# Kernel tuning notes

Measured on AMD Instinct MI355X. Metric: run time of the kernel, lower is better.

The kernel has to match this reference:

```python
import jax, jax.numpy as jnp
import numpy as np

N_NODES = 50000
N_EDGES = 150000
F_IN = 128
D = 512
N_GRAPHS = 256
BN_EPS = 1e-5


def setup_inputs() -> dict:
    key = jax.random.key(0)
    ks = jax.random.split(key, 16)
    x = jax.random.normal(ks[0], (N_NODES, F_IN), dtype=jnp.float32)
    edge_index = jax.random.randint(ks[1], (2, N_EDGES), 0, N_NODES, dtype=jnp.int64)
    batch = jnp.sort(jax.random.randint(ks[2], (N_NODES,), 0, N_GRAPHS, dtype=jnp.int64))
    # layer 1 MLP (F_IN -> D -> D)
    W1a = jax.random.normal(ks[3], (F_IN, D), dtype=jnp.float32) / np.sqrt(F_IN)
    b1a = jnp.zeros((D,), dtype=jnp.float32)
    W1b = jax.random.normal(ks[4], (D, D), dtype=jnp.float32) / np.sqrt(D)
    b1b = jnp.zeros((D,), dtype=jnp.float32)
    # layers 2-5 MLPs (D -> D -> D), stacked on leading axis
    Wa = jax.random.normal(ks[5], (4, D, D), dtype=jnp.float32) / np.sqrt(D)
    ba = jnp.zeros((4, D), dtype=jnp.float32)
    Wb = jax.random.normal(ks[6], (4, D, D), dtype=jnp.float32) / np.sqrt(D)
    bb = jnp.zeros((4, D), dtype=jnp.float32)
    # batchnorm affine params for the 5 BN layers
    gammas = jnp.ones((5, D), dtype=jnp.float32)
    betas = jnp.zeros((5, D), dtype=jnp.float32)
    # final fc
    fcW = jax.random.normal(ks[7], (D, D), dtype=jnp.float32) / np.sqrt(D)
    fcb = jnp.zeros((D,), dtype=jnp.float32)
    return {"x": x, "edge_index": edge_index, "batch": batch,
            "W1a": W1a, "b1a": b1a, "W1b": W1b, "b1b": b1b,
            "Wa": Wa, "ba": ba, "Wb": Wb, "bb": bb,
            "gammas": gammas, "betas": betas, "fcW": fcW, "fcb": fcb}


def _gin_block(x, src, dst, wa, ba_, wb, bb_, gamma, beta):
    # GINConv (eps=0): h_i = x_i + sum_{j->i} x_j, then 2-layer MLP
    agg = jnp.zeros_like(x).at[dst].add(x[src])
    h = x + agg
    h = jnp.maximum(h @ wa + ba_, 0.0) @ wb + bb_
    # outer ReLU then BatchNorm1d (training-mode batch stats, biased var)
    h = jnp.maximum(h, 0.0)
    mean = h.mean(axis=0)
    var = ((h - mean) ** 2).mean(axis=0)
    return gamma * (h - mean) * jax.lax.rsqrt(var + BN_EPS) + beta


def reference(x, edge_index, batch, W1a, b1a, W1b, b1b, Wa, ba, Wb, bb,
              gammas, betas, fcW, fcb):
    src, dst = edge_index[0], edge_index[1]
    h = _gin_block(x, src, dst, W1a, b1a, W1b, b1b, gammas[0], betas[0])
    for i in range(4):
        h = _gin_block(h, src, dst, Wa[i], ba[i], Wb[i], bb[i],
                       gammas[i + 1], betas[i + 1])
    # global mean pool over graphs
    sums = jax.ops.segment_sum(h, batch, num_segments=N_GRAPHS)
    counts = jax.ops.segment_sum(jnp.ones((h.shape[0],), dtype=h.dtype), batch,
                                 num_segments=N_GRAPHS)
    pooled = sums / jnp.maximum(counts, 1.0)[:, None]
    return jnp.tanh(pooled @ fcW + fcb)
```

## Files before the change

### kernel.cpp

```cpp
#include <hip/hip_runtime.h>
#include <math.h>

typedef unsigned short u16;
typedef unsigned int u32;
typedef __attribute__((ext_vector_type(8))) short bf16x8;
typedef __attribute__((ext_vector_type(4))) float f32x4;

__device__ __forceinline__ u16 f2bf(float x) {
    u32 u = __float_as_uint(x);
    return (u16)((u + 0x7FFFu + ((u >> 16) & 1u)) >> 16);
}
__device__ __forceinline__ float bf2f(u16 h) {
    return __uint_as_float(((u32)h) << 16);
}
__device__ __forceinline__ void async16(const void* g, void* l) {
    __builtin_amdgcn_global_load_lds((const __attribute__((address_space(1))) void*)g,
                                     (__attribute__((address_space(3))) void*)l,
                                     16, 0, 0);
}

__device__ __forceinline__ int idx_at(const void* p, long long i, int is64) {
    if (is64) return (int)((const long long*)p)[i];
    return ((const int*)p)[i];
}

__global__ void detect_kernel(const int* __restrict__ ei, int E, int* __restrict__ flag) {
    __shared__ int any;
    if (threadIdx.x == 0) any = 0;
    __syncthreads();
    int n = min(E, 1024);
    for (int i = threadIdx.x; i < n; i += blockDim.x)
        if (ei[2 * i + 1] != 0) any = 1;
    __syncthreads();
    if (threadIdx.x == 0) *flag = (any == 0) ? 1 : 0;
}

__global__ void hist_kernel(const void* __restrict__ idx, long long offs,
                            const int* __restrict__ flag,
                            int* __restrict__ cnt, int n) {
    int is64 = *flag;
    int i = blockIdx.x * blockDim.x + threadIdx.x;
    if (i < n) atomicAdd(&cnt[idx_at(idx, offs + i, is64)], 1);
}

__global__ void scan1_kernel(const int* __restrict__ cnt, int* __restrict__ ofs,
                             int* __restrict__ bsum, int n) {
    __shared__ int s[256];
    int b = blockIdx.x, t = threadIdx.x;
    int base = b * 1024 + t * 4;
    int v0 = (base + 0 < n) ? cnt[base + 0] : 0;
    int v1 = (base + 1 < n) ? cnt[base + 1] : 0;
    int v2 = (base + 2 < n) ? cnt[base + 2] : 0;
    int v3 = (base + 3 < n) ? cnt[base + 3] : 0;
    int tsum = v0 + v1 + v2 + v3;
    s[t] = tsum;
    __syncthreads();
    for (int off = 1; off < 256; off <<= 1) {
        int u = (t >= off) ? s[t - off] : 0;
        __syncthreads();
        s[t] += u;
        __syncthreads();
    }
    int pre = s[t] - tsum;
    int e0 = pre + v0, e1 = e0 + v1, e2 = e1 + v2, e3 = e2 + v3;
    if (base + 0 < n) ofs[base + 1] = e0;
    if (base + 1 < n) ofs[base + 2] = e1;
    if (base + 2 < n) ofs[base + 3] = e2;
    if (base + 3 < n) ofs[base + 4] = e3;
    if (t == 255) bsum[b] = s[255];
    if (b == 0 && t == 0) ofs[0] = 0;
}

__global__ void scan2_kernel(int* __restrict__ bsum, int nb) {
    int t = threadIdx.x;
    int orig = (t < nb) ? bsum[t] : 0;
    int v = orig;
    for (int d = 1; d < 64; d <<= 1) {
        int u = __shfl_up(v, d);
        if (t >= d) v += u;
    }
    if (t < nb) bsum[t] = v - orig;
}

__global__ void scan3_kernel(int* __restrict__ ofs, const int* __restrict__ bsum, int n) {
    int i = blockIdx.x * blockDim.x + threadIdx.x;
    if (i < n) ofs[i + 1] += bsum[i >> 10];
}

__global__ void fill_csr_kernel(const void* __restrict__ ei, long long E,
                                const int* __restrict__ flag,
                                int* __restrict__ cursor, int* __restrict__ esrc, int e) {
    int is64 = *flag;
    int i = blockIdx.x * blockDim.x + threadIdx.x;
    if (i < e) {
        int d = idx_at(ei, E + i, is64);
        int s = idx_at(ei, i, is64);
        int p = atomicAdd(&cursor[d], 1);
        esrc[p] = s;
    }
}

__global__ void copy_int_kernel(const int* __restrict__ a, int* __restrict__ b, int n) {
    int i = blockIdx.x * blockDim.x + threadIdx.x;
    if (i < n) b[i] = a[i];
}

__global__ void aggregate_split_kernel(const float* __restrict__ X,
                                       const int* __restrict__ row_ofs,
                                       const int* __restrict__ esrc,
                                       const float* __restrict__ scale,
                                       const float* __restrict__ shift,
                                       u16* __restrict__ Zhi, u16* __restrict__ Zlo,
                                       int n, int ncols) {
    int tpr = ncols >> 2;
    int nper = 256 / tpr;
    int node = blockIdx.x * nper + threadIdx.x / tpr;
    int c = (threadIdx.x % tpr) * 4;
    if (node >= n) return;
    int beg = row_ofs[node], end = row_ofs[node + 1];
    float4 acc = *reinterpret_cast<const float4*>(X + (size_t)node * ncols + c);
    int e = beg;
    for (; e + 1 < end; e += 2) {
        int s0 = esrc[e], s1 = esrc[e + 1];
        float4 a = *reinterpret_cast<const float4*>(X + (size_t)s0 * ncols + c);
        float4 b = *reinterpret_cast<const float4*>(X + (size_t)s1 * ncols + c);
        acc.x += a.x + b.x; acc.y += a.y + b.y;
        acc.z += a.z + b.z; acc.w += a.w + b.w;
    }
    if (e < end) {
        int s0 = esrc[e];
        float4 a = *reinterpret_cast<const float4*>(X + (size_t)s0 * ncols + c);
        acc.x += a.x; acc.y += a.y; acc.z += a.z; acc.w += a.w;
    }
    if (scale) {
        float d1 = (float)(end - beg + 1);
        float4 sc = *reinterpret_cast<const float4*>(scale + c);
        float4 sh = *reinterpret_cast<const float4*>(shift + c);
        acc.x = sc.x * acc.x + d1 * sh.x;
        acc.y = sc.y * acc.y + d1 * sh.y;
        acc.z = sc.z * acc.z + d1 * sh.z;
        acc.w = sc.w * acc.w + d1 * sh.w;
    }
    ushort4 hv, lv;
    hv.x = f2bf(acc.x); lv.x = f2bf(acc.x - bf2f(hv.x));
    hv.y = f2bf(acc.y); lv.y = f2bf(acc.y - bf2f(hv.y));
    hv.z = f2bf(acc.z); lv.z = f2bf(acc.z - bf2f(hv.z));
    hv.w = f2bf(acc.w); lv.w = f2bf(acc.w - bf2f(hv.w));
    *reinterpret_cast<ushort4*>(Zhi + (size_t)node * ncols + c) = hv;
    *reinterpret_cast<ushort4*>(Zlo + (size_t)node * ncols + c) = lv;
}

__global__ void transpose_split_kernel(const float* __restrict__ W, int K, int N,
                                       u16* __restrict__ Thi, u16* __restrict__ Tlo) {
    __shared__ float t[32][33];
    int k0 = blockIdx.x * 32, n0 = blockIdx.y * 32;
    int tx = threadIdx.x & 31, ty = threadIdx.x >> 5;
#pragma unroll
    for (int i = 0; i < 32; i += 8)
        t[ty + i][tx] = W[(size_t)(k0 + ty + i) * N + n0 + tx];
    __syncthreads();
#pragma unroll
    for (int i = 0; i < 32; i += 8) {
        float v = t[tx][ty + i];
        size_t o = (size_t)(n0 + ty + i) * K + k0 + tx;
        u16 h = f2bf(v);
        Thi[o] = h;
        Tlo[o] = f2bf(v - bf2f(h));
    }
}

struct TBatch {
    const float* src[10];
    u16* dh[10];
    u16* dl[10];
};
__global__ void transpose_split_batch_kernel(TBatch tb) {
    __shared__ float t[32][33];
    int z = blockIdx.z;
    const float* W = tb.src[z];
    u16* Thi = tb.dh[z];
    u16* Tlo = tb.dl[z];
    int k0 = blockIdx.x * 32, n0 = blockIdx.y * 32;
    int tx = threadIdx.x & 31, ty = threadIdx.x >> 5;
#pragma unroll
    for (int i = 0; i < 32; i += 8)
        t[ty + i][tx] = W[(size_t)(k0 + ty + i) * 512 + n0 + tx];
    __syncthreads();
#pragma unroll
    for (int i = 0; i < 32; i += 8) {
        float v = t[tx][ty + i];
        size_t o = (size_t)(n0 + ty + i) * 512 + k0 + tx;
        u16 h = f2bf(v);
        Thi[o] = h;
        Tlo[o] = f2bf(v - bf2f(h));
    }
}

template <int MODE>
__global__ __launch_bounds__(256, 4)
void gemm_mfma(const u16* __restrict__ Ahi, const u16* __restrict__ Alo,
               const u16* __restrict__ Bhi, const u16* __restrict__ Blo,
               const float* __restrict__ bias, int M, int K, int mblk,
               u16* __restrict__ Ohi, u16* __restrict__ Olo,
               float* __restrict__ Of32, float* __restrict__ stats) {
    __shared__ __align__(16) char lds[32768];
    char* ldsAhi = lds;
    char* ldsAlo = lds + 8192;
    char* ldsBhi = lds + 16384;
    char* ldsBlo = lds + 24576;

    const int bid = blockIdx.x;
    const int mt = (bid >> 5) * 8 + (bid & 7);
    const int nb = (bid & 31) >> 3;
    if (mt >= mblk) return;
    const int row0 = mt * 128;
    const int col0 = nb * 128;

    const int tid = threadIdx.x;
    const int lane = tid & 63;
    const int wave = tid >> 6;
    const int wr = wave >> 1, wc = wave & 1;

    f32x4 acc[4][4];
#pragma unroll
    for (int mi = 0; mi < 4; ++mi)
#pragma unroll
        for (int ni = 0; ni < 4; ++ni)
            acc[mi][ni] = (f32x4){0.f, 0.f, 0.f, 0.f};

    const int nkt = K >> 5;
    for (int kt = 0; kt < nkt; ++kt) {
        const int k0 = kt << 5;
#pragma unroll
        for (int i = 0; i < 2; ++i) {
            int c = tid + i * 256;
            int row = c >> 2, s = c & 3;
            int ks = ((s ^ (row & 3)) << 3);
            int ar = row0 + row; if (ar > M - 1) ar = M - 1;
            size_t aoff = (size_t)ar * K + k0 + ks;
            size_t boff = (size_t)(col0 + row) * K + k0 + ks;
            async16(Ahi + aoff, ldsAhi + c * 16);
            async16(Alo + aoff, ldsAlo + c * 16);
            async16(Bhi + boff, ldsBhi + c * 16);
            async16(Blo + boff, ldsBlo + c * 16);
        }
        __syncthreads();
        {
            bf16x8 ah[4], al[4], bh[4], bl[4];
            const int kc = lane >> 4;
#pragma unroll
            for (int mi = 0; mi < 4; ++mi) {
                int ml = wr * 64 + mi * 16 + (lane & 15);
                int off = ml * 64 + ((kc ^ (ml & 3)) << 4);
                ah[mi] = *(const bf16x8*)(ldsAhi + off);
                al[mi] = *(const bf16x8*)(ldsAlo + off);
            }
#pragma unroll
            for (int ni = 0; ni < 4; ++ni) {
                int nl = wc * 64 + ni * 16 + (lane & 15);
                int off = nl * 64 + ((kc ^ (nl & 3)) << 4);
                bh[ni] = *(const bf16x8*)(ldsBhi + off);
                bl[ni] = *(const bf16x8*)(ldsBlo + off);
            }
#pragma unroll
            for (int mi = 0; mi < 4; ++mi)
#pragma unroll
                for (int ni = 0; ni < 4; ++ni) {
                    acc[mi][ni] = __builtin_amdgcn_mfma_f32_16x16x32_bf16(
                        ah[mi], bh[ni], acc[mi][ni], 0, 0, 0);
                    acc[mi][ni] = __builtin_amdgcn_mfma_f32_16x16x32_bf16(
                        ah[mi], bl[ni], acc[mi][ni], 0, 0, 0);
                    acc[mi][ni] = __builtin_amdgcn_mfma_f32_16x16x32_bf16(
                        al[mi], bh[ni], acc[mi][ni], 0, 0, 0);
                }
        }
        __syncthreads();
    }

    const int cl = lane & 15;
    const int rb = (lane >> 4) * 4;
    if (MODE == 0) {
#pragma unroll
        for (int ni = 0; ni < 4; ++ni) {
            int gc = col0 + wc * 64 + ni * 16 + cl;
            float bv = bias[gc];
#pragma unroll
            for (int mi = 0; mi < 4; ++mi) {
                int gr0 = row0 + wr * 64 + mi * 16 + rb;
#pragma unroll
                for (int r = 0; r < 4; ++r) {
                    int gr = gr0 + r;
                    if (gr < M) {
                        float v = fmaxf(acc[mi][ni][r] + bv, 0.f);
                        u16 h = f2bf(v);
                        Ohi[(size_t)gr * 512 + gc] = h;
                        Olo[(size_t)gr * 512 + gc] = f2bf(v - bf2f(h));
                    }
                }
            }
        }
    } else {
#pragma unroll
        for (int ni = 0; ni < 4; ++ni) {
            int gc = col0 + wc * 64 + ni * 16 + cl;
            float bv = bias[gc];
            float s = 0.f, q = 0.f;
#pragma unroll
            for (int mi = 0; mi < 4; ++mi) {
                int gr0 = row0 + wr * 64 + mi * 16 + rb;
#pragma unroll
                for (int r = 0; r < 4; ++r) {
                    int gr = gr0 + r;
                    if (gr < M) {
                        float v = fmaxf(acc[mi][ni][r] + bv, 0.f);
                        Of32[(size_t)gr * 512 + gc] = v;
                        s += v; q += v * v;
                    }
                }
            }
            s += __shfl_xor(s, 16); s += __shfl_xor(s, 32);
            q += __shfl_xor(q, 16); q += __shfl_xor(q, 32);
            if (lane < 16) {
                atomicAdd(&stats[gc], s);
                atomicAdd(&stats[512 + gc], q);
            }
        }
    }
}

__global__ void bn_params_kernel(const float* __restrict__ stats,
                                 const float* __restrict__ gamma,
                                 const float* __restrict__ beta,
                                 float* __restrict__ scale, float* __restrict__ shift,
                                 float invN) {
    int c = blockIdx.x * blockDim.x + threadIdx.x;
    if (c >= 512) return;
    float mean = stats[c] * invN;
    float var = fmaxf(stats[512 + c] * invN - mean * mean, 0.f);
    float a = gamma[c] * rsqrtf(var + 1e-5f);
    scale[c] = a;
    shift[c] = beta[c] - mean * a;
}

#define POOL_ROWS 64
__global__ void pool_kernel(const float* __restrict__ H, const void* __restrict__ batch,
                            const int* __restrict__ flag,
                            float* __restrict__ pooled, int n) {
    int is64 = *flag;
    int c = threadIdx.x * 4;
    int r0 = blockIdx.x * POOL_ROWS;
    if (r0 >= n) return;
    int r1 = min(r0 + POOL_ROWS, n);
    int g = idx_at(batch, r0, is64);
    float4 acc = make_float4(0.f, 0.f, 0.f, 0.f);
    for (int r = r0; r < r1; ++r) {
        int gr = idx_at(batch, r, is64);
        if (gr != g) {
            atomicAdd(&pooled[(size_t)g * 512 + c + 0], acc.x);
            atomicAdd(&pooled[(size_t)g * 512 + c + 1], acc.y);
            atomicAdd(&pooled[(size_t)g * 512 + c + 2], acc.z);
            atomicAdd(&pooled[(size_t)g * 512 + c + 3], acc.w);
            acc = make_float4(0.f, 0.f, 0.f, 0.f);
            g = gr;
        }
        float4 v = *reinterpret_cast<const float4*>(H + (size_t)r * 512 + c);
        acc.x += v.x; acc.y += v.y; acc.z += v.z; acc.w += v.w;
    }
    atomicAdd(&pooled[(size_t)g * 512 + c + 0], acc.x);
    atomicAdd(&pooled[(size_t)g * 512 + c + 1], acc.y);
    atomicAdd(&pooled[(size_t)g * 512 + c + 2], acc.z);
    atomicAdd(&pooled[(size_t)g * 512 + c + 3], acc.w);
}

__global__ void finalize_pool_kernel(const float* __restrict__ pooled,
                                     const int* __restrict__ cg,
                                     const float* __restrict__ scale,
                                     const float* __restrict__ shift,
                                     float* __restrict__ Apool, int total) {
    int idx = blockIdx.x * blockDim.x + threadIdx.x;
    if (idx >= total) return;
    int g = idx >> 9;
    int c = idx & 511;
    float cnt = fmaxf((float)cg[g], 1.f);
    Apool[idx] = scale[c] * (pooled[idx] / cnt) + shift[c];
}

__global__ void fc_tanh_kernel(const float* __restrict__ A,
                               const u16* __restrict__ WThi, const u16* __restrict__ WTlo,
                               const float* __restrict__ bias,
                               float* __restrict__ out, int G) {
    int tm = threadIdx.x >> 6;
    int tn = threadIdx.x & 63;
    int m = blockIdx.x * 4 + tm;
    int n = blockIdx.y * 64 + tn;
    if (m >= G) return;
    const float* a = A + (size_t)m * 512;
    const u16* wh = WThi + (size_t)n * 512;
    const u16* wl = WTlo + (size_t)n * 512;
    float acc = 0.f;
    for (int k = 0; k < 512; k += 4) {
        float4 av = *reinterpret_cast<const float4*>(a + k);
        ushort4 h4 = *reinterpret_cast<const ushort4*>(wh + k);
        ushort4 l4 = *reinterpret_cast<const ushort4*>(wl + k);
        acc += av.x * (bf2f(h4.x) + bf2f(l4.x));
        acc += av.y * (bf2f(h4.y) + bf2f(l4.y));
        acc += av.z * (bf2f(h4.z) + bf2f(l4.z));
        acc += av.w * (bf2f(h4.w) + bf2f(l4.w));
    }
    out[(size_t)m * 512 + n] = tanhf(acc + bias[n]);
}

extern "C" void kernel_launch(void* const* d_in, const int* in_sizes, int n_in,
                              void* d_out, int out_size, void* d_ws, size_t ws_size,
                              hipStream_t stream) {
    const float* x      = (const float*)d_in[0];
    const void*  ei     = d_in[1];
    const void*  batch  = d_in[2];
    const float* W1a    = (const float*)d_in[3];
    const float* b1a    = (const float*)d_in[4];
    const float* W1b    = (const float*)d_in[5];
    const float* b1b    = (const float*)d_in[6];
    const float* Wa     = (const float*)d_in[7];
    const float* ba     = (const float*)d_in[8];
    const float* Wb     = (const float*)d_in[9];
    const float* bb     = (const float*)d_in[10];
    const float* gammas = (const float*)d_in[11];
    const float* betas  = (const float*)d_in[12];
    const float* fcW    = (const float*)d_in[13];
    const float* fcb    = (const float*)d_in[14];

    const int N = in_sizes[2];
    const int E = in_sizes[1] / 2;
    const int F = in_sizes[0] / N;
    const int G = out_size / 512;

    char* w = (char*)d_ws;
    size_t off = 0;
    auto alloc = [&](size_t bytes) -> void* {
        void* p = w + off;
        off = (off + bytes + 255) & ~(size_t)255;
        return p;
    };
    float* slotA  = (float*)alloc((size_t)N * 512 * 4);
    float* slotB  = (float*)alloc((size_t)N * 512 * 4);
    int*   row_ofs= (int*)alloc((size_t)(N + 1) * 4);
    int*   cnt    = (int*)alloc((size_t)N * 4);
    int*   esrc   = (int*)alloc((size_t)E * 4);
    int*   cg     = (int*)alloc((size_t)G * 4);
    int*   bsum   = (int*)alloc(256 * 4);
    float* stats  = (float*)alloc(1024 * 4);
    float* scale  = (float*)alloc(512 * 4);
    float* shift  = (float*)alloc(512 * 4);
    float* pooled = (float*)alloc((size_t)G * 512 * 4);
    float* Apool  = (float*)alloc((size_t)G * 512 * 4);
    int*   flag   = (int*)alloc(256);
    const size_t WSZ = (size_t)512 * 512;
    u16* g1h[5]; u16* g1l[5]; u16* g2h[5]; u16* g2l[5];
    for (int i = 0; i < 5; ++i) {
        g1h[i] = (u16*)alloc(WSZ * 2); g1l[i] = (u16*)alloc(WSZ * 2);
        g2h[i] = (u16*)alloc(WSZ * 2); g2l[i] = (u16*)alloc(WSZ * 2);
    }
    u16* fch = (u16*)alloc(WSZ * 2); u16* fcl = (u16*)alloc(WSZ * 2);
    (void)ws_size; (void)n_in;

    {
        dim3 gK128(128 / 32, 512 / 32);
        transpose_split_kernel<<<gK128, 256, 0, stream>>>(W1a, 128, 512, g1h[0], g1l[0]);
        TBatch tb;
        tb.src[0] = W1b; tb.dh[0] = g2h[0]; tb.dl[0] = g2l[0];
        for (int i = 0; i < 4; ++i) {
            tb.src[1 + i] = Wa + (size_t)i * WSZ; tb.dh[1 + i] = g1h[i + 1]; tb.dl[1 + i] = g1l[i + 1];
            tb.src[5 + i] = Wb + (size_t)i * WSZ; tb.dh[5 + i] = g2h[i + 1]; tb.dl[5 + i] = g2l[i + 1];
        }
        tb.src[9] = fcW; tb.dh[9] = fch; tb.dl[9] = fcl;
        dim3 gB(16, 16, 10);
        transpose_split_batch_kernel<<<gB, 256, 0, stream>>>(tb);
    }

    detect_kernel<<<1, 256, 0, stream>>>((const int*)ei, E, flag);
    hipMemsetAsync(cnt, 0, (size_t)N * 4, stream);
    hist_kernel<<<(E + 255) / 256, 256, 0, stream>>>(ei, (long long)E, flag, cnt, E);
    int nb = (N + 1023) / 1024;
    scan1_kernel<<<nb, 256, 0, stream>>>(cnt, row_ofs, bsum, N);
    scan2_kernel<<<1, 64, 0, stream>>>(bsum, nb);
    scan3_kernel<<<(N + 255) / 256, 256, 0, stream>>>(row_ofs, bsum, N);
    copy_int_kernel<<<(N + 255) / 256, 256, 0, stream>>>(row_ofs, cnt, N);
    fill_csr_kernel<<<(E + 255) / 256, 256, 0, stream>>>(ei, (long long)E, flag, cnt, esrc, E);
    hipMemsetAsync(cg, 0, (size_t)G * 4, stream);
    hist_kernel<<<(N + 255) / 256, 256, 0, stream>>>(batch, 0, flag, cg, N);

    const float* curH = x;
    float* zslot = slotA;
    float* tslot = slotB;
    int ncols = F;
    const float* scaleP = nullptr;
    const float* shiftP = nullptr;
    const int mblk = (N + 127) / 128;
    const int ngrp = (mblk + 7) / 8;
    dim3 ggrid(ngrp * 32);

    for (int L = 0; L < 5; ++L) {
        u16* Zhi = (u16*)zslot; u16* Zlo = Zhi + (size_t)N * 512;
        u16* Thi = (u16*)tslot; u16* Tlo = Thi + (size_t)N * 512;
        float* H = zslot;

        int tpr = ncols / 4;
        int nper = 256 / tpr;
        aggregate_split_kernel<<<(N + nper - 1) / nper, 256, 0, stream>>>(
            curH, row_ofs, esrc, scaleP, shiftP, Zhi, Zlo, N, ncols);

        const float* ba_ = (L == 0) ? b1a : ba + (size_t)(L - 1) * 512;
        const float* bb_ = (L == 0) ? b1b : bb + (size_t)(L - 1) * 512;

        gemm_mfma<0><<<ggrid, 256, 0, stream>>>(Zhi, Zlo, g1h[L], g1l[L], ba_,
                                                N, ncols, mblk, Thi, Tlo, nullptr, nullptr);
        hipMemsetAsync(stats, 0, 1024 * 4, stream);
        gemm_mfma<1><<<ggrid, 256, 0, stream>>>(Thi, Tlo, g2h[L], g2l[L], bb_,
                                                N, 512, mblk, nullptr, nullptr, H, stats);
        bn_params_kernel<<<2, 256, 0, stream>>>(stats, gammas + (size_t)L * 512,
                                                betas + (size_t)L * 512,
                                                scale, shift, 1.f / (float)N);
        curH = H;
        ncols = 512;
        scaleP = scale;
        shiftP = shift;
        float* tmp = zslot; zslot = tslot; tslot = tmp;
    }
    const float* Hfin = curH;

    hipMemsetAsync(pooled, 0, (size_t)G * 512 * 4, stream);
    pool_kernel<<<(N + POOL_ROWS - 1) / POOL_ROWS, 128, 0, stream>>>(Hfin, batch, flag, pooled, N);
    int total = G * 512;
    finalize_pool_kernel<<<(total + 255) / 256, 256, 0, stream>>>(pooled, cg, scale, shift,
                                                                  Apool, total);

    dim3 fgrid((G + 3) / 4, 512 / 64);
    fc_tanh_kernel<<<fgrid, 256, 0, stream>>>(Apool, fch, fcl, fcb, (float*)d_out, G);
}
```

Baseline: 1.572 ms.

## Double-buffer GEMM LDS tiles with BK=64 and 8 waves per block

Restructures the split-bf16 MFMA GEMM to use 512 threads (8 waves, each computing 64x32) and a K-tile of 64. The hi/lo halves are interleaved in one swizzled LDS layout, and two buffers let the next tile's async global->LDS loads overlap the current tile's MFMAs. It also raises wave priority around the MFMA bursts. The cost is 128KB of LDS per block, which limits occupancy to one block per CU. The one barrier per iteration may not be enough to guarantee the async loads have landed before they are read.

```diff
diff --git a/kernel.cpp b/kernel.cpp
--- a/kernel.cpp
+++ b/kernel.cpp
@@ -197,75 +197,84 @@
 }
 
 template <int MODE>
-__global__ __launch_bounds__(256, 4)
+__global__ __launch_bounds__(512, 2)
 void gemm_mfma(const u16* __restrict__ Ahi, const u16* __restrict__ Alo,
                const u16* __restrict__ Bhi, const u16* __restrict__ Blo,
                const float* __restrict__ bias, int M, int K, int mblk,
                u16* __restrict__ Ohi, u16* __restrict__ Olo,
                float* __restrict__ Of32, float* __restrict__ stats) {
-    __shared__ __align__(16) char lds[32768];
-    char* ldsAhi = lds;
-    char* ldsAlo = lds + 8192;
-    char* ldsBhi = lds + 16384;
-    char* ldsBlo = lds + 24576;
+    __shared__ __align__(16) char lds[131072];
 
     const int bid = blockIdx.x;
     const int mt = (bid >> 5) * 8 + (bid & 7);
-    const int nb = (bid & 31) >> 3;
+    const int nbk = (bid & 31) >> 3;
     if (mt >= mblk) return;
     const int row0 = mt * 128;
-    const int col0 = nb * 128;
+    const int col0 = nbk * 128;
 
     const int tid = threadIdx.x;
     const int lane = tid & 63;
     const int wave = tid >> 6;
-    const int wr = wave >> 1, wc = wave & 1;
-
-    f32x4 acc[4][4];
+    const int wr = wave >> 2, wc = wave & 3;
+
+    f32x4 acc[4][2];
 #pragma unroll
     for (int mi = 0; mi < 4; ++mi)
 #pragma unroll
-        for (int ni = 0; ni < 4; ++ni)
+        for (int ni = 0; ni < 2; ++ni)
             acc[mi][ni] = (f32x4){0.f, 0.f, 0.f, 0.f};
 
-    const int nkt = K >> 5;
+    auto stage = [&](int buf, int kt) {
+        char* ldsA = lds + buf * 65536;
+        char* ldsB = ldsA + 32768;
+        const int k0 = kt << 6;
+#pragma unroll
+        for (int i = 0; i < 4; ++i) {
+            int lin = tid + i * 512;
+            int row = lin >> 4, p = lin & 15;
+            int c = p ^ (row & 15);
+            int eo = (c & 7) * 8;
+            int ar = row0 + row; if (ar > M - 1) ar = M - 1;
+            const u16* asrc = (c < 8 ? Ahi : Alo) + (size_t)ar * K + k0 + eo;
+            async16(asrc, ldsA + lin * 16);
+            const u16* bsrc = (c < 8 ? Bhi : Blo) + (size_t)(col0 + row) * K + k0 + eo;
+            async16(bsrc, ldsB + lin * 16);
+        }
+    };
+
+    const int nkt = K >> 6;
+    stage(0, 0);
+    __syncthreads();
+
+    int cur = 0;
     for (int kt = 0; kt < nkt; ++kt) {
-        const int k0 = kt << 5;
-#pragma unroll
-        for (int i = 0; i < 2; ++i) {
-            int c = tid + i * 256;
-            int row = c >> 2, s = c & 3;
-            int ks = ((s ^ (row & 3)) << 3);
-            int ar = row0 + row; if (ar > M - 1) ar = M - 1;
-            size_t aoff = (size_t)ar * K + k0 + ks;
-            size_t boff = (size_t)(col0 + row) * K + k0 + ks;
-            async16(Ahi + aoff, ldsAhi + c * 16);
-            async16(Alo + aoff, ldsAlo + c * 16);
-            async16(Bhi + boff, ldsBhi + c * 16);
-            async16(Blo + boff, ldsBlo + c * 16);
-        }
-        __syncthreads();
-        {
-            bf16x8 ah[4], al[4], bh[4], bl[4];
+        if (kt + 1 < nkt) stage(cur ^ 1, kt + 1);
+        char* ldsA = lds + cur * 65536;
+        char* ldsB = ldsA + 32768;
+#pragma unroll
+        for (int kk = 0; kk < 2; ++kk) {
+            bf16x8 ah[4], al[4], bh[2], bl[2];
             const int kc = lane >> 4;
+            const int chi = kk * 4 + kc;
 #pragma unroll
             for (int mi = 0; mi < 4; ++mi) {
                 int ml = wr * 64 + mi * 16 + (lane & 15);
-                int off = ml * 64 + ((kc ^ (ml & 3)) << 4);
-                ah[mi] = *(const bf16x8*)(ldsAhi + off);
-                al[mi] = *(const bf16x8*)(ldsAlo + off);
+                const char* base = ldsA + ml * 256;
+                ah[mi] = *(const bf16x8*)(base + ((chi ^ (ml & 15)) << 4));
+                al[mi] = *(const bf16x8*)(base + (((chi + 8) ^ (ml & 15)) << 4));
             }
 #pragma unroll
-            for (int ni = 0; ni < 4; ++ni) {
-                int nl = wc * 64 + ni * 16 + (lane & 15);
-                int off = nl * 64 + ((kc ^ (nl & 3)) << 4);
-                bh[ni] = *(const bf16x8*)(ldsBhi + off);
-                bl[ni] = *(const bf16x8*)(ldsBlo + off);
+            for (int ni = 0; ni < 2; ++ni) {
+                int nl = wc * 32 + ni * 16 + (lane & 15);
+                const char* base = ldsB + nl * 256;
+                bh[ni] = *(const bf16x8*)(base + ((chi ^ (nl & 15)) << 4));
+                bl[ni] = *(const bf16x8*)(base + (((chi + 8) ^ (nl & 15)) << 4));
             }
+            __builtin_amdgcn_s_setprio(1);
 #pragma unroll
             for (int mi = 0; mi < 4; ++mi)
 #pragma unroll
-                for (int ni = 0; ni < 4; ++ni) {
+                for (int ni = 0; ni < 2; ++ni) {
                     acc[mi][ni] = __builtin_amdgcn_mfma_f32_16x16x32_bf16(
                         ah[mi], bh[ni], acc[mi][ni], 0, 0, 0);
                     acc[mi][ni] = __builtin_amdgcn_mfma_f32_16x16x32_bf16(
@@ -273,16 +282,18 @@
                     acc[mi][ni] = __builtin_amdgcn_mfma_f32_16x16x32_bf16(
                         al[mi], bh[ni], acc[mi][ni], 0, 0, 0);
                 }
+            __builtin_amdgcn_s_setprio(0);
         }
         __syncthreads();
+        cur ^= 1;
     }
 
     const int cl = lane & 15;
     const int rb = (lane >> 4) * 4;
     if (MODE == 0) {
 #pragma unroll
-        for (int ni = 0; ni < 4; ++ni) {
-            int gc = col0 + wc * 64 + ni * 16 + cl;
+        for (int ni = 0; ni < 2; ++ni) {
+            int gc = col0 + wc * 32 + ni * 16 + cl;
             float bv = bias[gc];
 #pragma unroll
             for (int mi = 0; mi < 4; ++mi) {
@@ -301,8 +312,8 @@
         }
     } else {
 #pragma unroll
-        for (int ni = 0; ni < 4; ++ni) {
-            int gc = col0 + wc * 64 + ni * 16 + cl;
+        for (int ni = 0; ni < 2; ++ni) {
+            int gc = col0 + wc * 32 + ni * 16 + cl;
             float bv = bias[gc];
             float s = 0.f, q = 0.f;
 #pragma unroll
@@ -512,10 +523,10 @@
         const float* ba_ = (L == 0) ? b1a : ba + (size_t)(L - 1) * 512;
         const float* bb_ = (L == 0) ? b1b : bb + (size_t)(L - 1) * 512;
 
-        gemm_mfma<0><<<ggrid, 256, 0, stream>>>(Zhi, Zlo, g1h[L], g1l[L], ba_,
+        gemm_mfma<0><<<ggrid, 512, 0, stream>>>(Zhi, Zlo, g1h[L], g1l[L], ba_,
                                                 N, ncols, mblk, Thi, Tlo, nullptr, nullptr);
         hipMemsetAsync(stats, 0, 1024 * 4, stream);
-        gemm_mfma<1><<<ggrid, 256, 0, stream>>>(Thi, Tlo, g2h[L], g2l[L], bb_,
+        gemm_mfma<1><<<ggrid, 512, 0, stream>>>(Thi, Tlo, g2h[L], g2l[L], bb_,
                                                 N, 512, mblk, nullptr, nullptr, H, stats);
         bn_params_kernel<<<2, 256, 0, stream>>>(stats, gammas + (size_t)L * 512,
                                                 betas + (size_t)L * 512,
```

After: 1.703 ms. 8.3% more time.
